# Kernel tuning notes

Hardware: AMD Instinct MI355X
Metric: run time of the kernel (lower is better)

Reference implementation:

```python
import jax, jax.numpy as jnp
import numpy as np

B, D, V = 1024, 512, 100000
M = 0.4
EPS = 1e-07


def setup_inputs() -> dict:
    key = jax.random.key(0)
    k1, k2, k3 = jax.random.split(key, 3)
    inp = jax.random.normal(k1, (B, D), dtype=jnp.float32)
    # xavier_uniform for (D, V): limit = sqrt(6/(D+V))
    limit = float(np.sqrt(6.0 / (D + V)))
    weight = jax.random.uniform(k2, (D, V), dtype=jnp.float32, minval=-limit, maxval=limit)
    labels = jax.random.randint(k3, (B,), 0, V, dtype=jnp.int64)
    return {"input": inp, "weight": weight, "labels": labels}


def reference(input, weight, labels):
    # L2-normalize rows of input and columns of weight (F.normalize eps=1e-12)
    x_norm = input / jnp.maximum(jnp.linalg.norm(input, axis=1, keepdims=True), 1e-12)
    w_norm = weight / jnp.maximum(jnp.linalg.norm(weight, axis=0, keepdims=True), 1e-12)
    cosine = x_norm @ w_norm                                # [B, V]
    cosine = jnp.clip(cosine, -1.0 + EPS, 1.0 - EPS)
    arcos = jnp.arccos(cosine)
    # add margin m only at the label class (one-hot add without dense one-hot)
    rows = jnp.arange(B)
    arcos = arcos.at[rows, labels].add(M)
    logits = jnp.cos(arcos)                                 # [B, V]
    # cross-entropy, mean reduction
    logz = jax.nn.logsumexp(logits, axis=1)                 # [B]
    label_logit = logits[rows, labels]                      # [B]
    loss = jnp.mean(logz - label_logit)
    return loss
```

## Files before the change

### kernel.cpp

```cpp
#include <hip/hip_runtime.h>
#include <hip/hip_bf16.h>
#include <math.h>

#define B_    1024
#define D_    512
#define V_    100000
#define NT_   782
#define EPS_  1e-7f
#define COSM  0.9210609940028851f
#define SINM  0.3894183423086505f

typedef __bf16 bf16x8 __attribute__((ext_vector_type(8)));
typedef float  f32x4  __attribute__((ext_vector_type(4)));

struct alignas(16) US8 { unsigned short h[8]; };

__device__ __forceinline__ unsigned short f2bf(float f) {
  union { float f; unsigned u; } a; a.f = f;
  unsigned u = a.u;
  u += 0x7FFFu + ((u >> 16) & 1u);
  return (unsigned short)(u >> 16);
}

__device__ __forceinline__ void async_copy16(void* lds, const void* g) {
  __builtin_amdgcn_global_load_lds(
      (const __attribute__((address_space(1))) void*)g,
      (__attribute__((address_space(3))) void*)lds, 16, 0, 0);
}

__global__ void x_prep(const float* __restrict__ x,
                       unsigned short* __restrict__ xb,
                       float* __restrict__ S) {
  int t = threadIdx.x;
  int lane = t & 63, wave = t >> 6;
  int row = blockIdx.x * 4 + wave;
  const float* xr = x + (size_t)row * D_;
  f32x4 a = *(const f32x4*)(xr + lane * 8);
  f32x4 b = *(const f32x4*)(xr + lane * 8 + 4);
  float ss = a[0]*a[0] + a[1]*a[1] + a[2]*a[2] + a[3]*a[3]
           + b[0]*b[0] + b[1]*b[1] + b[2]*b[2] + b[3]*b[3];
#pragma unroll
  for (int off = 32; off > 0; off >>= 1) ss += __shfl_xor(ss, off, 64);
  float inv = 1.0f / fmaxf(sqrtf(ss), 1e-12f);
  US8 pk;
#pragma unroll
  for (int j = 0; j < 4; ++j) pk.h[j]     = f2bf(a[j] * inv);
#pragma unroll
  for (int j = 0; j < 4; ++j) pk.h[4 + j] = f2bf(b[j] * inv);
  *(US8*)(xb + (size_t)row * D_ + lane * 8) = pk;
  if (lane == 0) S[row] = 0.0f;
}

#define BM 128
#define BN 128
#define BK 64

__global__ __launch_bounds__(256) void gemm_fused(
    const unsigned short* __restrict__ xb,
    const float* __restrict__ w,
    const int* __restrict__ labels,
    float* __restrict__ S, float* __restrict__ Lb) {
  int bid = blockIdx.x;
  int xcd = bid & 7;
  int slot = bid >> 3;
  int tn = xcd * 98 + (slot >> 3);
  int tm = slot & 7;
  if (tn >= NT_) return;
  int m0 = tm * BM, n0 = tn * BN;

  __shared__ unsigned short Ab[BM * BK];
  __shared__ unsigned short Bb[BN * BK];
  __shared__ float sqred[8][BN];
  __shared__ float iwL[BN];
  __shared__ int labT[BM];
  int t = threadIdx.x;
  if (t < BM) labT[t] = labels[m0 + t];
  int lane = t & 63;
  int q = lane >> 4, l15 = lane & 15;
  int wave = t >> 6;
  int wm = (wave & 1) * 64, wn = (wave >> 1) * 64;
  f32x4 acc[4][4] = {};

  const unsigned short* gA[4];
  unsigned short* lA[4];
#pragma unroll
  for (int j = 0; j < 4; ++j) {
    int p = t + 256 * j;
    int m = p >> 3;
    int kc = (p & 7) ^ (m & 7);
    gA[j] = xb + (size_t)(m0 + m) * D_ + kc * 8;
    lA[j] = Ab + p * 8;
  }

  int cg = t & 31;
  int rp = t >> 5;
  int c0l = cg * 4;
  bool vok = (n0 + c0l + 3) < V_;
  const float* wbase = w + (size_t)rp * 8 * V_ + n0 + c0l;
  unsigned short* bdst[4];
#pragma unroll
  for (int cc = 0; cc < 4; ++cc) {
    int col = c0l + cc;
    bdst[cc] = &Bb[(col * 8 + (rp ^ (col & 7))) * 8];
  }
  float ssq[4] = {0.0f, 0.0f, 0.0f, 0.0f};

  for (int kt = 0; kt < D_; kt += BK) {
#pragma unroll
    for (int j = 0; j < 4; ++j) async_copy16(lA[j], gA[j] + kt);

    f32x4 row[8];
    if (vok) {
#pragma unroll
      for (int i = 0; i < 8; ++i)
        row[i] = *(const f32x4*)(wbase + (size_t)i * V_);
    } else {
#pragma unroll
      for (int i = 0; i < 8; ++i) row[i] = f32x4{0.0f, 0.0f, 0.0f, 0.0f};
    }
#pragma unroll
    for (int cc = 0; cc < 4; ++cc) {
      US8 pk;
#pragma unroll
      for (int i = 0; i < 8; ++i) {
        float v = row[i][cc];
        ssq[cc] += v * v;
        pk.h[i] = f2bf(v);
      }
      *(US8*)bdst[cc] = pk;
    }
    wbase += (size_t)BK * V_;

    __syncthreads();
    int h = l15 & 7;
#pragma unroll
    for (int s = 0; s < 2; ++s) {
      int kx = s * 4 + q;
      bf16x8 af[4], bfr[4];
#pragma unroll
      for (int ri = 0; ri < 4; ++ri) {
        int row_ = wm + ri * 16 + l15;
        af[ri] = *(const bf16x8*)&Ab[(row_ * 8 + (kx ^ h)) * 8];
      }
#pragma unroll
      for (int ci = 0; ci < 4; ++ci) {
        int row_ = wn + ci * 16 + l15;
        bfr[ci] = *(const bf16x8*)&Bb[(row_ * 8 + (kx ^ h)) * 8];
      }
#pragma unroll
      for (int ri = 0; ri < 4; ++ri)
#pragma unroll
        for (int ci = 0; ci < 4; ++ci)
          acc[ri][ci] = __builtin_amdgcn_mfma_f32_16x16x32_bf16(
              af[ri], bfr[ci], acc[ri][ci], 0, 0, 0);
    }
    __syncthreads();
  }

#pragma unroll
  for (int cc = 0; cc < 4; ++cc) sqred[rp][c0l + cc] = ssq[cc];
  __syncthreads();
  if (t < BN) {
    float tot = 0.0f;
#pragma unroll
    for (int p = 0; p < 8; ++p) tot += sqred[p][t];
    iwL[t] = ((n0 + t) < V_) ? 1.0f / fmaxf(sqrtf(tot), 1e-12f) : 0.0f;
  }
  __syncthreads();

  float iw[4]; int vcol[4];
#pragma unroll
  for (int ci = 0; ci < 4; ++ci) {
    int nl = wn + ci * 16 + l15;
    vcol[ci] = n0 + nl;
    iw[ci] = iwL[nl];
  }
#pragma unroll
  for (int ri = 0; ri < 4; ++ri) {
#pragma unroll
    for (int reg = 0; reg < 4; ++reg) {
      int ml = wm + ri * 16 + q * 4 + reg;
      int r = m0 + ml;
      int lab = labT[ml];
      float s = 0.0f;
#pragma unroll
      for (int ci = 0; ci < 4; ++ci) {
        float cv = acc[ri][ci][reg] * iw[ci];
        cv = fminf(fmaxf(cv, -1.0f + EPS_), 1.0f - EPS_);
        float logit = cv;
        if (vcol[ci] == lab) {
          logit = cv * COSM - sqrtf(fmaxf(1.0f - cv * cv, 0.0f)) * SINM;
          Lb[r] = logit;
        }
        s += (vcol[ci] < V_) ? __expf(logit) : 0.0f;
      }
      s += __shfl_xor(s, 1, 64);
      s += __shfl_xor(s, 2, 64);
      s += __shfl_xor(s, 4, 64);
      s += __shfl_xor(s, 8, 64);
      if (l15 == 0) atomicAdd(&S[r], s);
    }
  }
}

__global__ void finalk(const float* __restrict__ S, const float* __restrict__ Lb,
                       float* __restrict__ out) {
  __shared__ float red[256];
  int t = threadIdx.x;
  float s = 0.0f;
  for (int i = t; i < B_; i += 256) s += logf(S[i]) - Lb[i];
  red[t] = s;
  __syncthreads();
  for (int o = 128; o > 0; o >>= 1) {
    if (t < o) red[t] += red[t + o];
    __syncthreads();
  }
  if (t == 0) out[0] = red[0] * (1.0f / B_);
}

extern "C" void kernel_launch(void* const* d_in, const int* in_sizes, int n_in,
                              void* d_out, int out_size, void* d_ws, size_t ws_size,
                              hipStream_t stream) {
  const float* x = (const float*)d_in[0];
  const float* w = (const float*)d_in[1];
  const int* labels = (const int*)d_in[2];
  float* out = (float*)d_out;
  char* ws = (char*)d_ws;
  unsigned short* xb = (unsigned short*)ws;
  float* S  = (float*)(ws + 1048576ull);
  float* Lb = (float*)(ws + 1052672ull);

  x_prep<<<256, 256, 0, stream>>>(x, xb, S);
  gemm_fused<<<6272, 256, 0, stream>>>(xb, w, labels, S, Lb);
  finalk<<<1, 256, 0, stream>>>(S, Lb, out);
}
```

Baseline: 517.3 us.

## Prefetch half of next weight tile before MFMA and rotate LDS store order

Splits each thread's 8-row weight load into two halves, issuing the first half for the next k-step right after the barrier so it overlaps the MFMA work, while the second half is loaded at the top of the iteration. It also rotates the column store order per thread pair to spread LDS bank accesses during the bf16 packing writes. The aim is to hide global-memory latency for the fp32 weight stream, at the cost of extra live registers that may reduce occupancy.

After: 536.7 us. 3.8% more time.

```diff
diff --git a/kernel.cpp b/kernel.cpp
--- a/kernel.cpp
+++ b/kernel.cpp
@@ -96,42 +96,63 @@
   int rp = t >> 5;
   int c0l = cg * 4;
   bool vok = (n0 + c0l + 3) < V_;
-  const float* wbase = w + (size_t)rp * 8 * V_ + n0 + c0l;
-  unsigned short* bdst[4];
-#pragma unroll
-  for (int cc = 0; cc < 4; ++cc) {
-    int col = c0l + cc;
-    bdst[cc] = &Bb[(col * 8 + (rp ^ (col & 7))) * 8];
-  }
+  const float* wb = w + (size_t)rp * 8 * V_ + n0 + c0l;
+  int ccrot = (t >> 1) & 3;
   float ssq[4] = {0.0f, 0.0f, 0.0f, 0.0f};
 
+  f32x4 lo[4];
+  if (vok) {
+#pragma unroll
+    for (int i = 0; i < 4; ++i) lo[i] = *(const f32x4*)(wb + (size_t)i * V_);
+  } else {
+#pragma unroll
+    for (int i = 0; i < 4; ++i) lo[i] = f32x4{0.0f, 0.0f, 0.0f, 0.0f};
+  }
+
   for (int kt = 0; kt < D_; kt += BK) {
+    f32x4 hi[4];
+    if (vok) {
+#pragma unroll
+      for (int i = 0; i < 4; ++i)
+        hi[i] = *(const f32x4*)(wb + (size_t)(4 + i) * V_);
+    } else {
+#pragma unroll
+      for (int i = 0; i < 4; ++i) hi[i] = f32x4{0.0f, 0.0f, 0.0f, 0.0f};
+    }
 #pragma unroll
     for (int j = 0; j < 4; ++j) async_copy16(lA[j], gA[j] + kt);
 
-    f32x4 row[8];
-    if (vok) {
-#pragma unroll
-      for (int i = 0; i < 8; ++i)
-        row[i] = *(const f32x4*)(wbase + (size_t)i * V_);
-    } else {
-#pragma unroll
-      for (int i = 0; i < 8; ++i) row[i] = f32x4{0.0f, 0.0f, 0.0f, 0.0f};
-    }
-#pragma unroll
-    for (int cc = 0; cc < 4; ++cc) {
+#pragma unroll
+    for (int j = 0; j < 4; ++j) {
+      int cc = (j + ccrot) & 3;
+      int col = c0l + cc;
       US8 pk;
 #pragma unroll
-      for (int i = 0; i < 8; ++i) {
-        float v = row[i][cc];
+      for (int i = 0; i < 4; ++i) {
+        float v = lo[i][cc];
         ssq[cc] += v * v;
         pk.h[i] = f2bf(v);
       }
-      *(US8*)bdst[cc] = pk;
-    }
-    wbase += (size_t)BK * V_;
-
+#pragma unroll
+      for (int i = 0; i < 4; ++i) {
+        float v = hi[i][cc];
+        ssq[cc] += v * v;
+        pk.h[4 + i] = f2bf(v);
+      }
+      *(US8*)&Bb[(col * 8 + (rp ^ (col & 7))) * 8] = pk;
+    }
     __syncthreads();
+
+    const float* wbn = wb + (size_t)BK * V_;
+    if (kt + BK < D_) {
+      if (vok) {
+#pragma unroll
+        for (int i = 0; i < 4; ++i)
+          lo[i] = *(const f32x4*)(wbn + (size_t)i * V_);
+      }
+    }
+    wb = wbn;
+
     int h = l15 & 7;
 #pragma unroll
     for (int s = 0; s < 2; ++s) {
```
